# Performance work log

Hardware: AMD Instinct MI355X
Metric: run time of the kernel (lower is better)

The kernel has to match this reference:

```python
import jax, jax.numpy as jnp
import numpy as np
from jax import lax

LATENT = 128
CODEBOOK = 1024

def _conv(x, w, b):
    # NCHW conv, kernel OIHW, stride 1, padding 1 (same)
    y = lax.conv_general_dilated(x, w, (1, 1), ((1, 1), (1, 1)),
                                 dimension_numbers=('NCHW', 'OIHW', 'NCHW'))
    return y + b[None, :, None, None]

def _conv_transpose(x, w, b):
    # ConvTranspose2d(k=3, s=1, p=1) == conv with flipped kernel, in/out swapped, pad 1
    w_eff = jnp.flip(w, (2, 3)).transpose(1, 0, 2, 3)  # [Cin,Cout,3,3] -> [Cout,Cin,3,3]
    return _conv(x, w_eff, b)

def _maxpool2(x):
    return lax.reduce_window(x, -jnp.inf, lax.max, (1, 1, 2, 2), (1, 1, 2, 2), 'VALID')

def _upsample2(x):
    # F.interpolate(scale_factor=2), default nearest
    return jnp.repeat(jnp.repeat(x, 2, axis=2), 2, axis=3)

def setup_inputs() -> dict:
    key = jax.random.key(0)
    ks = jax.random.split(key, 20)
    f = jnp.float32
    inp = {
        'x': jax.random.uniform(ks[0], (8192, 1, 24, 24), dtype=f),
        'conv1_w': jax.random.normal(ks[1], (32, 1, 3, 3), f) * 0.1,
        'conv1_b': jnp.zeros((32,), f),
        'conv2_w': jax.random.normal(ks[2], (64, 32, 3, 3), f) * 0.05,
        'conv2_b': jnp.zeros((64,), f),
        'conv3_w': jax.random.normal(ks[3], (128, 64, 3, 3), f) * 0.04,
        'conv3_b': jnp.zeros((128,), f),
        'enc_fc_w': jax.random.normal(ks[4], (LATENT, 3 * 3 * 128), f) * 0.03,
        'enc_fc_b': jnp.zeros((LATENT,), f),
        'codebook': jax.random.normal(ks[5], (CODEBOOK, LATENT), f),
        'dec_fc_w': jax.random.normal(ks[6], (3 * 3 * 128, LATENT), f) * 0.09,
        'dec_fc_b': jnp.zeros((3 * 3 * 128,), f),
        'dct1_w': jax.random.normal(ks[7], (128, 64, 3, 3), f) * 0.03,  # [Cin,Cout,kh,kw]
        'dct1_b': jnp.zeros((64,), f),
        'dct2_w': jax.random.normal(ks[8], (64, 32, 3, 3), f) * 0.04,
        'dct2_b': jnp.zeros((32,), f),
        'dct3_w': jax.random.normal(ks[9], (32, 1, 3, 3), f) * 0.06,
        'dct3_b': jnp.zeros((1,), f),
    }
    return inp

def reference(x, conv1_w, conv1_b, conv2_w, conv2_b, conv3_w, conv3_b,
              enc_fc_w, enc_fc_b, codebook, dec_fc_w, dec_fc_b,
              dct1_w, dct1_b, dct2_w, dct2_b, dct3_w, dct3_b):
    # ---- Encoder ----
    h = _maxpool2(jax.nn.relu(_conv(x, conv1_w, conv1_b)))     # [B,32,12,12]
    h = _maxpool2(jax.nn.relu(_conv(h, conv2_w, conv2_b)))     # [B,64,6,6]
    h = _maxpool2(jax.nn.relu(_conv(h, conv3_w, conv3_b)))     # [B,128,3,3]
    z = h.reshape(-1, 3 * 3 * 128) @ enc_fc_w.T + enc_fc_b     # [B,128]
    # ---- Quantize (L2 nearest-codeword; matmul-trick distances, same argmin) ----
    d2 = (jnp.sum(z * z, axis=1, keepdims=True)
          - 2.0 * z @ codebook.T
          + jnp.sum(codebook * codebook, axis=1)[None, :])     # [B,K]
    idx = jnp.argmin(d2, axis=1)                               # [B]
    z_q = codebook[idx]                                        # [B,128]
    # ---- Decoder ----
    d = z_q @ dec_fc_w.T + dec_fc_b                            # [B,1152]
    d = d.reshape(-1, 128, 3, 3)
    d = _upsample2(jax.nn.relu(_conv_transpose(d, dct1_w, dct1_b)))  # [B,64,6,6]
    d = _upsample2(jax.nn.relu(_conv_transpose(d, dct2_w, dct2_b)))  # [B,32,12,12]
    d = _upsample2(jax.nn.relu(_conv_transpose(d, dct3_w, dct3_b)))  # [B,1,24,24]
    return d
```

## Files before the change

kernel.cpp:

```cpp
#include <hip/hip_runtime.h>

typedef __attribute__((ext_vector_type(8))) short short8;
typedef __attribute__((ext_vector_type(4))) float f32x4;
typedef unsigned short ushort_t;
typedef unsigned int uint_t;

#define OFF_W1R   0
#define OFF_BD2F  288
#define OFF_BD1F  18720
#define OFF_EWT   (18720+73728)
#define OFF_CT    (92448+147456)
#define OFF_CC    (239904+131072)
#define OFF_DWT   (370976+1024)
#define OFF_D1R   (372000+147456)
#define OFF_D3R   (593184+18432)
#define WS_WEIGHTS (611616+288)
#define OFF_W2BF  WS_WEIGHTS
#define OFF_W3BF  (OFF_W2BF+18432)
#define OFF_H     (OFF_W3BF+73728)
#define OFF_TABLE OFF_H
#define OFF_IDSN  (OFF_H+8192*1152)

__device__ __forceinline__ ushort_t f2bf(float v) {
  uint_t u = __float_as_uint(v);
  return (ushort_t)((u + 0x7FFFu + ((u >> 16) & 1u)) >> 16);
}
__device__ __forceinline__ float bf2f(ushort_t b) {
  return __uint_as_float(((uint_t)b) << 16);
}

#define P2_N (92160 + 294912 + 262144 + 73728 + 18432)
#define PREP_N (WS_WEIGHTS + P2_N)
__global__ void vq_prep_all(const float* __restrict__ conv1_w, const float* __restrict__ conv2_w,
                            const float* __restrict__ conv3_w, const float* __restrict__ enc_fc_w,
                            const float* __restrict__ codebook, const float* __restrict__ dec_fc_w,
                            const float* __restrict__ dct1_w, const float* __restrict__ dct2_w,
                            const float* __restrict__ dct3_w, float* __restrict__ ws) {
  int i0 = blockIdx.x * blockDim.x + threadIdx.x;
  if (i0 >= PREP_N) return;
  if (i0 < WS_WEIGHTS) {
    int i = i0;
    if (i < OFF_BD2F) {
      int tap = i >> 5, co = i & 31;
      ws[i] = conv1_w[co*9 + tap];
    } else if (i < OFF_CC) {
      return;
    } else if (i < OFF_DWT) {
      int k = i - OFF_CC;
      float s = 0.f;
      for (int j = 0; j < 128; ++j) { float v = codebook[k*128+j]; s += v*v; }
      ws[i] = s;
    } else if (i < OFF_D1R) {
      int l = i - OFF_DWT;
      int j = l % 1152, k = l / 1152;
      ws[i] = dec_fc_w[j*128 + k];
    } else if (i < OFF_D3R) {
      return;
    } else {
      int l = i - OFF_D3R;
      int tap = l % 9, ci = l / 9;
      ws[i] = dct3_w[ci*9 + (8 - tap)];
    }
    return;
  }
  int i = i0 - WS_WEIGHTS;
  ushort_t* W2  = (ushort_t*)(ws + OFF_W2BF);
  ushort_t* W3  = (ushort_t*)(ws + OFF_W3BF);
  ushort_t* EW  = (ushort_t*)(ws + OFF_EWT);
  ushort_t* CB  = (ushort_t*)(ws + OFF_CT);
  ushort_t* BD1 = (ushort_t*)(ws + OFF_BD1F);
  ushort_t* BD2 = (ushort_t*)(ws + OFF_BD2F);
  if (i < 18432) {
    int tap = i >> 11, r = i & 2047, co = r >> 5, ch = r & 31;
    float v = conv2_w[(co*32 + ch)*9 + tap];
    ushort_t hb = f2bf(v);
    W2[i] = hb; W2[18432 + i] = f2bf(v - bf2f(hb));
  } else if (i < 92160) {
    int j = i - 18432;
    int tap = j >> 13, r = j & 8191, co = r >> 6, ch = r & 63;
    float v = conv3_w[(co*64 + ch)*9 + tap];
    ushort_t hb = f2bf(v);
    W3[j] = hb; W3[73728 + j] = f2bf(v - bf2f(hb));
  } else if (i < 387072) {
    int r = i - 92160;
    int p = r / 147456; r %= 147456;
    int kk = r & 31, n = (r >> 5) & 127, ks = r >> 12;
    float v = enc_fc_w[n*1152 + ks*32 + kk];
    ushort_t hb = f2bf(v);
    if (p == 0) EW[r] = hb; else EW[147456 + r] = f2bf(v - bf2f(hb));
  } else if (i < 649216) {
    int r = i - 387072;
    int p = r / 131072; r %= 131072;
    int kk = r & 31, cw = (r >> 5) & 1023, ks = r >> 15;
    float v = codebook[cw*128 + ks*32 + kk];
    ushort_t hb = f2bf(v);
    if (p == 0) CB[r] = hb; else CB[131072 + r] = f2bf(v - bf2f(hb));
  } else if (i < 722944) {
    int r = i - 649216;
    int co = r / 1152, k = r - co*1152;
    int tap = k >> 7, ci = k & 127;
    float v = dct1_w[(ci*64 + co)*9 + (8 - tap)];
    ushort_t hb = f2bf(v);
    BD1[r] = hb; BD1[73728 + r] = f2bf(v - bf2f(hb));
  } else {
    int r = i - 722944;
    int co = r / 576, k = r - co*576;
    int tap = k >> 6, ci = k & 63;
    float v = dct2_w[(ci*32 + co)*9 + (8 - tap)];
    ushort_t hb = f2bf(v);
    BD2[r] = hb; BD2[18432 + r] = f2bf(v - bf2f(hb));
  }
}

__global__ __launch_bounds__(256, 4) void vq_enc(
    const float* __restrict__ x,
    const float* __restrict__ b1, const float* __restrict__ b2, const float* __restrict__ b3,
    const float* __restrict__ ws, ushort_t* __restrict__ hhi, ushort_t* __restrict__ hlo)
{
  __shared__ ushort_t R0h[7840], R0l[7840];
  __shared__ float XT[624];
  ushort_t* C3h = R0h;
  ushort_t* C3l = R0l;
  const int t = threadIdx.x;
  const int b = blockIdx.x;

  for (int i = t; i < 3920; i += 256) { ((uint_t*)R0h)[i] = 0u; ((uint_t*)R0l)[i] = 0u; }
  const float* xb = x + (size_t)b * 576;
  for (int i = t; i < 624; i += 256) {
    int row = i / 26, col = i - row * 26;
    XT[i] = (col >= 1 && col <= 24) ? xb[row*24 + col - 1] : 0.f;
  }
  __syncthreads();

  {
    int co = t & 31, g = t >> 5, gy = g >> 1, gx = g & 1;
    float w[9];
    #pragma unroll
    for (int k = 0; k < 9; ++k) w[k] = ws[OFF_W1R + k*32 + co];
    float bias = b1[co];
    #pragma unroll
    for (int pr = 0; pr < 3; ++pr) {
      int Y = gy*6 + pr*2;
      float a0[12], a1[12];
      #pragma unroll
      for (int i = 0; i < 12; ++i) { a0[i] = 0.f; a1[i] = 0.f; }
      #pragma unroll
      for (int wy = 0; wy < 4; ++wy) {
        int ry = Y - 1 + wy;
        if (ry < 0 || ry > 23) continue;
        const float2* rp = (const float2*)&XT[ry*26 + gx*12];
        float r[14];
        #pragma unroll
        for (int k = 0; k < 7; ++k) { float2 p = rp[k]; r[2*k] = p.x; r[2*k+1] = p.y; }
        if (wy < 3) {
          #pragma unroll
          for (int xx = 0; xx < 12; ++xx)
            #pragma unroll
            for (int dx = 0; dx < 3; ++dx) a0[xx] += r[xx+dx] * w[wy*3+dx];
        }
        if (wy >= 1) {
          #pragma unroll
          for (int xx = 0; xx < 12; ++xx)
            #pragma unroll
            for (int dx = 0; dx < 3; ++dx) a1[xx] += r[xx+dx] * w[(wy-1)*3+dx];
        }
      }
      #pragma unroll
      for (int pc = 0; pc < 6; ++pc) {
        float m = fmaxf(fmaxf(a0[2*pc], a0[2*pc+1]), fmaxf(a1[2*pc], a1[2*pc+1]));
        float v = m + bias; v = v > 0.f ? v : 0.f;
        int row = gy*3 + pr, colp = gx*6 + pc;
        int addr = ((row+1)*14 + (colp+1))*40 + co;
        ushort_t hb = f2bf(v);
        R0h[addr] = hb;
        R0l[addr] = f2bf(v - bf2f(hb));
      }
    }
  }
  __syncthreads();

  const int lane = t & 63, quad = lane >> 4, col = lane & 15;
  const int wv = t >> 6;

  {
    const int h = wv & 1, p = wv >> 1;
    const ushort_t* W2 = (const ushort_t*)(ws + OFF_W2BF);
    int baseA[5];
    #pragma unroll
    for (int mi = 0; mi < 5; ++mi) {
      int m = (h*5 + mi)*16 + col; if (m > 143) m = 143;
      int cell = m >> 2, sub = m & 3;
      int opy = cell / 6, opx = cell - opy*6;
      int y = 2*opy + (sub >> 1), xx = 2*opx + (sub & 1);
      baseA[mi] = (y*14 + xx)*40 + quad*8;
    }
    f32x4 acc[5][2];
    #pragma unroll
    for (int mi = 0; mi < 5; ++mi) { acc[mi][0] = (f32x4)0.f; acc[mi][1] = (f32x4)0.f; }
    const int co0 = p*32 + col, co1 = co0 + 16;
    #pragma unroll
    for (int t9 = 0; t9 < 9; ++t9) {
      const int TAPOFF = ((t9/3)*14 + (t9%3))*40;
      int bidx = t9*2048 + quad*8;
      short8 Bh0 = *(const short8*)(W2 + bidx + co0*32);
      short8 Bh1 = *(const short8*)(W2 + bidx + co1*32);
      short8 Bl0 = *(const short8*)(W2 + 18432 + bidx + co0*32);
      short8 Bl1 = *(const short8*)(W2 + 18432 + bidx + co1*32);
      #pragma unroll
      for (int mi = 0; mi < 5; ++mi) {
        int a = baseA[mi] + TAPOFF;
        short8 Ah = *(const short8*)(R0h + a);
        short8 Al = *(const short8*)(R0l + a);
        acc[mi][0] = __builtin_amdgcn_mfma_f32_16x16x32_bf16(Al, Bh0, acc[mi][0], 0, 0, 0);
        acc[mi][0] = __builtin_amdgcn_mfma_f32_16x16x32_bf16(Ah, Bl0, acc[mi][0], 0, 0, 0);
        acc[mi][0] = __builtin_amdgcn_mfma_f32_16x16x32_bf16(Ah, Bh0, acc[mi][0], 0, 0, 0);
        acc[mi][1] = __builtin_amdgcn_mfma_f32_16x16x32_bf16(Al, Bh1, acc[mi][1], 0, 0, 0);
        acc[mi][1] = __builtin_amdgcn_mfma_f32_16x16x32_bf16(Ah, Bl1, acc[mi][1], 0, 0, 0);
        acc[mi][1] = __builtin_amdgcn_mfma_f32_16x16x32_bf16(Ah, Bh1, acc[mi][1], 0, 0, 0);
      }
    }
    __syncthreads();
    for (int i = t; i < 2304; i += 256) { ((uint_t*)C3h)[i] = 0u; ((uint_t*)C3l)[i] = 0u; }
    __syncthreads();
    #pragma unroll
    for (int mi = 0; mi < 5; ++mi) {
      int cell = (h*5 + mi)*4 + quad;
      if (cell < 36) {
        int opy = cell / 6, opx = cell - opy*6;
        int wa = ((opy+1)*8 + (opx+1))*72;
        #pragma unroll
        for (int j = 0; j < 2; ++j) {
          int ch = j ? co1 : co0;
          f32x4 a = acc[mi][j];
          float v = fmaxf(fmaxf(a.x, a.y), fmaxf(a.z, a.w)) + b2[ch];
          v = v > 0.f ? v : 0.f;
          ushort_t hb = f2bf(v);
          C3h[wa + ch] = hb;
          C3l[wa + ch] = f2bf(v - bf2f(hb));
        }
      }
    }
  }
  __syncthreads();

  {
    const ushort_t* W3 = (const ushort_t*)(ws + OFF_W3BF);
    int baseA[3];
    #pragma unroll
    for (int mt = 0; mt < 3; ++mt) {
      int m = mt*16 + col; if (m > 35) m = 35;
      int cell = m >> 2, sub = m & 3;
      int opy = cell / 3, opx = cell - opy*3;
      int y = 2*opy + (sub >> 1), xx = 2*opx + (sub & 1);
      baseA[mt] = (y*8 + xx)*72 + quad*8;
    }
    f32x4 acc[3][2];
    #pragma unroll
    for (int mt = 0; mt < 3; ++mt) { acc[mt][0] = (f32x4)0.f; acc[mt][1] = (f32x4)0.f; }
    const int co0 = wv*16 + col, co1 = co0 + 64;
    #pragma unroll
    for (int ks = 0; ks < 18; ++ks) {
      const int t9 = ks >> 1, ch0 = (ks & 1)*32;
      const int TAPOFF = ((t9/3)*8 + (t9%3))*72;
      int bidx = t9*8192 + ch0 + quad*8;
      short8 Bh0 = *(const short8*)(W3 + bidx + co0*64);
      short8 Bh1 = *(const short8*)(W3 + bidx + co1*64);
      short8 Bl0 = *(const short8*)(W3 + 73728 + bidx + co0*64);
      short8 Bl1 = *(const short8*)(W3 + 73728 + bidx + co1*64);
      #pragma unroll
      for (int mt = 0; mt < 3; ++mt) {
        int a = baseA[mt] + TAPOFF + ch0;
        short8 Ah = *(const short8*)(C3h + a);
        short8 Al = *(const short8*)(C3l + a);
        acc[mt][0] = __builtin_amdgcn_mfma_f32_16x16x32_bf16(Al, Bh0, acc[mt][0], 0, 0, 0);
        acc[mt][0] = __builtin_amdgcn_mfma_f32_16x16x32_bf16(Ah, Bl0, acc[mt][0], 0, 0, 0);
        acc[mt][0] = __builtin_amdgcn_mfma_f32_16x16x32_bf16(Ah, Bh0, acc[mt][0], 0, 0, 0);
        acc[mt][1] = __builtin_amdgcn_mfma_f32_16x16x32_bf16(Al, Bh1, acc[mt][1], 0, 0, 0);
        acc[mt][1] = __builtin_amdgcn_mfma_f32_16x16x32_bf16(Ah, Bl1, acc[mt][1], 0, 0, 0);
        acc[mt][1] = __builtin_amdgcn_mfma_f32_16x16x32_bf16(Ah, Bh1, acc[mt][1], 0, 0, 0);
      }
    }
    ushort_t* hb_ = hhi + (size_t)b * 1152;
    ushort_t* lb_ = hlo + (size_t)b * 1152;
    #pragma unroll
    for (int mt = 0; mt < 3; ++mt) {
      int cell = mt*4 + quad;
      if (cell < 9) {
        #pragma unroll
        for (int j = 0; j < 2; ++j) {
          int ch = j ? co1 : co0;
          f32x4 a = acc[mt][j];
          float v = fmaxf(fmaxf(a.x, a.y), fmaxf(a.z, a.w)) + b3[ch];
          v = v > 0.f ? v : 0.f;
          ushort_t hb2 = f2bf(v);
          hb_[ch*9 + cell] = hb2;
          lb_[ch*9 + cell] = f2bf(v - bf2f(hb2));
        }
      }
    }
  }
}

__global__ __launch_bounds__(256, 4) void vq_fc_argmin(
    const float* __restrict__ efb, const float* __restrict__ ws,
    const ushort_t* __restrict__ hhi, const ushort_t* __restrict__ hlo,
    int* __restrict__ ids)
{
  __shared__ float ZL[16*132];
  __shared__ float WVs[64];
  __shared__ int   WIs[64];
  const int t = threadIdx.x;
  const int sb = blockIdx.x * 16;
  const int lane = t & 63, wv = t >> 6;
  const int col = lane & 15, quad = lane >> 4;

  const ushort_t* EW  = (const ushort_t*)(ws + OFF_EWT);
  const ushort_t* CBB = (const ushort_t*)(ws + OFF_CT);

  f32x4 acc0 = (f32x4)0.f, acc1 = (f32x4)0.f;
  const size_t hrow = (size_t)(sb + col) * 1152 + quad*8;
  #pragma unroll 4
  for (int ks = 0; ks < 36; ++ks) {
    short8 Ah = *(const short8*)(hhi + hrow + ks*32);
    short8 Al = *(const short8*)(hlo + hrow + ks*32);
    int n0 = wv*32 + col, n1 = n0 + 16;
    const ushort_t* bp0 = EW + (ks*128 + n0)*32 + quad*8;
    const ushort_t* bp1 = EW + (ks*128 + n1)*32 + quad*8;
    short8 Bh0 = *(const short8*)(bp0);
    short8 Bl0 = *(const short8*)(bp0 + 147456);
    short8 Bh1 = *(const short8*)(bp1);
    short8 Bl1 = *(const short8*)(bp1 + 147456);
    acc0 = __builtin_amdgcn_mfma_f32_16x16x32_bf16(Al, Bh0, acc0, 0, 0, 0);
    acc0 = __builtin_amdgcn_mfma_f32_16x16x32_bf16(Ah, Bl0, acc0, 0, 0, 0);
    acc0 = __builtin_amdgcn_mfma_f32_16x16x32_bf16(Ah, Bh0, acc0, 0, 0, 0);
    acc1 = __builtin_amdgcn_mfma_f32_16x16x32_bf16(Al, Bh1, acc1, 0, 0, 0);
    acc1 = __builtin_amdgcn_mfma_f32_16x16x32_bf16(Ah, Bl1, acc1, 0, 0, 0);
    acc1 = __builtin_amdgcn_mfma_f32_16x16x32_bf16(Ah, Bh1, acc1, 0, 0, 0);
  }
  {
    int n0 = wv*32 + col, n1 = n0 + 16;
    float bs0 = efb[n0], bs1 = efb[n1];
    #pragma unroll
    for (int r = 0; r < 4; ++r) {
      int m = quad*4 + r;
      ZL[m*132 + n0] = acc0[r] + bs0;
      ZL[m*132 + n1] = acc1[r] + bs1;
    }
  }
  __syncthreads();

  short8 zAh[4], zAl[4];
  #pragma unroll
  for (int ks = 0; ks < 4; ++ks) {
    const float* zp = &ZL[col*132 + ks*32 + quad*8];
    float4 z0 = *(const float4*)zp;
    float4 z1 = *(const float4*)(zp + 4);
    float zv[8] = {z0.x, z0.y, z0.z, z0.w, z1.x, z1.y, z1.z, z1.w};
    ushort_t ph[8], pl[8];
    #pragma unroll
    for (int e = 0; e < 8; ++e) {
      ushort_t hb = f2bf(zv[e]);
      ph[e] = hb; pl[e] = f2bf(zv[e] - bf2f(hb));
    }
    zAh[ks] = *(const short8*)ph;
    zAl[ks] = *(const short8*)pl;
  }

  float bestv[4]; int besti[4];
  #pragma unroll
  for (int r = 0; r < 4; ++r) { bestv[r] = 3.4e38f; besti[r] = 0; }
  for (int c4 = 0; c4 < 4; ++c4) {
    f32x4 dacc[4];
    #pragma unroll
    for (int nn = 0; nn < 4; ++nn) dacc[nn] = (f32x4)0.f;
    #pragma unroll
    for (int ks = 0; ks < 4; ++ks) {
      #pragma unroll
      for (int nn = 0; nn < 4; ++nn) {
        int cw = (wv*16 + c4*4 + nn)*16 + col;
        const ushort_t* bp = CBB + (size_t)(ks*1024 + cw)*32 + quad*8;
        short8 Bh = *(const short8*)bp;
        short8 Bl = *(const short8*)(bp + 131072);
        dacc[nn] = __builtin_amdgcn_mfma_f32_16x16x32_bf16(zAl[ks], Bh, dacc[nn], 0, 0, 0);
        dacc[nn] = __builtin_amdgcn_mfma_f32_16x16x32_bf16(zAh[ks], Bl, dacc[nn], 0, 0, 0);
        dacc[nn] = __builtin_amdgcn_mfma_f32_16x16x32_bf16(zAh[ks], Bh, dacc[nn], 0, 0, 0);
      }
    }
    #pragma unroll
    for (int nn = 0; nn < 4; ++nn) {
      int cw = (wv*16 + c4*4 + nn)*16 + col;
      float ccv = ws[OFF_CC + cw];
      #pragma unroll
      for (int r = 0; r < 4; ++r) {
        float dist = ccv - 2.f*dacc[nn][r];
        if (dist < bestv[r]) { bestv[r] = dist; besti[r] = cw; }
      }
    }
  }

  #pragma unroll
  for (int r = 0; r < 4; ++r) {
    float v = bestv[r]; int ii = besti[r];
    #pragma unroll
    for (int off = 8; off >= 1; off >>= 1) {
      float v2 = __shfl_xor(v, off); int i2 = __shfl_xor(ii, off);
      if (v2 < v || (v2 == v && i2 < ii)) { v = v2; ii = i2; }
    }
    if (col == 0) {
      int m = quad*4 + r;
      WVs[wv*16 + m] = v; WIs[wv*16 + m] = ii;
    }
  }
  __syncthreads();
  if (t < 16) {
    float v = WVs[t]; int ii = WIs[t];
    #pragma unroll
    for (int w2 = 1; w2 < 4; ++w2) {
      float v2 = WVs[w2*16 + t]; int i2 = WIs[w2*16 + t];
      if (v2 < v || (v2 == v && i2 < ii)) { v = v2; ii = i2; }
    }
    ids[sb + t] = ii;
  }
}

__global__ __launch_bounds__(256, 4) void vq_dec_table(
    const float* __restrict__ codebook, const float* __restrict__ decb,
    const float* __restrict__ d1b, const float* __restrict__ d2b, const float* __restrict__ d3b,
    const float* __restrict__ ws, float* __restrict__ table)
{
  __shared__ float POOL[8008];
  __shared__ float PS[1536];
  __shared__ float ZQ[128];
  ushort_t* FAh = (ushort_t*)POOL;
  ushort_t* FAl = FAh + 3400;
  ushort_t* GAh = (ushort_t*)(POOL + 3400);
  ushort_t* GAl = GAh + 4608;
  float* R2 = POOL;

  const int t = threadIdx.x;
  const int cw = blockIdx.x;
  const int lane = t & 63, wv = t >> 6;
  const int col = lane & 15, quad = lane >> 4;

  for (int i = t; i < 8008; i += 256) POOL[i] = 0.f;
  if (t < 128) ZQ[t] = codebook[(size_t)cw*128 + t];
  __syncthreads();

  #pragma unroll
  for (int p = 0; p < 5; ++p) {
    int j = t + p*256;
    if (j < 1152) {
      float a0 = decb[j];
      const float* wb = ws + OFF_DWT + j;
      #pragma unroll 4
      for (int k = 0; k < 128; ++k) a0 += wb[k*1152] * ZQ[k];
      int ci = j / 9, rem = j - ci*9;
      int pix = ((rem/3)+1)*5 + (rem%3) + 1;
      ushort_t hb = f2bf(a0);
      FAh[pix*136 + ci] = hb;
      FAl[pix*136 + ci] = f2bf(a0 - bf2f(hb));
    }
  }
  __syncthreads();

  const ushort_t* BD1 = (const ushort_t*)(ws + OFF_BD1F);
  f32x4 acc1 = (f32x4)0.f;
  {
    const int m9 = col < 9 ? col : 8;
    const int oy = m9/3, ox = m9 - oy*3;
    const int co = wv*16 + col;
    #pragma unroll 4
    for (int ks = 0; ks < 36; ++ks) {
      int kb = ks*32 + quad*8;
      int tap = kb >> 7, ci0 = kb & 127;
      int pix = (oy + tap/3)*5 + ox + tap%3;
      short8 Ah = *(const short8*)(FAh + pix*136 + ci0);
      short8 Al = *(const short8*)(FAl + pix*136 + ci0);
      const ushort_t* bp = BD1 + co*1152 + kb;
      short8 Bh = *(const short8*)bp;
      short8 Bl = *(const short8*)(bp + 73728);
      acc1 = __builtin_amdgcn_mfma_f32_16x16x32_bf16(Al, Bh, acc1, 0, 0, 0);
      acc1 = __builtin_amdgcn_mfma_f32_16x16x32_bf16(Ah, Bl, acc1, 0, 0, 0);
      acc1 = __builtin_amdgcn_mfma_f32_16x16x32_bf16(Ah, Bh, acc1, 0, 0, 0);
    }
  }
  {
    const int co = wv*16 + col;
    float bias = d1b[co];
    #pragma unroll
    for (int r = 0; r < 4; ++r) {
      int m = quad*4 + r;
      if (m < 9) {
        int oy = m/3, ox = m - oy*3;
        float v = acc1[r] + bias; v = v > 0.f ? v : 0.f;
        ushort_t hb = f2bf(v), lb = f2bf(v - bf2f(hb));
        int rbase = (2*oy+1)*8 + (2*ox+1);
        GAh[(rbase  )*72 + co] = hb; GAh[(rbase+1)*72 + co] = hb;
        GAh[(rbase+8)*72 + co] = hb; GAh[(rbase+9)*72 + co] = hb;
        GAl[(rbase  )*72 + co] = lb; GAl[(rbase+1)*72 + co] = lb;
        GAl[(rbase+8)*72 + co] = lb; GAl[(rbase+9)*72 + co] = lb;
      }
    }
  }
  __syncthreads();

  const ushort_t* BD2 = (const ushort_t*)(ws + OFF_BD2F);
  f32x4 acc2[3];
  acc2[0] = (f32x4)0.f; acc2[1] = (f32x4)0.f; acc2[2] = (f32x4)0.f;
  const int h = wv >> 1, js = (wv & 1)*3;
  for (int ks = h*9; ks < h*9 + 9; ++ks) {
    int kb = ks*32 + quad*8;
    int tap = kb >> 6, ci0 = kb & 63;
    int ty = tap/3, tx = tap - ty*3;
    #pragma unroll
    for (int jj = 0; jj < 3; ++jj) {
      int job = js + jj;
      int mt = job >> 1, nt = job & 1;
      int m = mt*16 + col; if (m > 35) m = 35;
      int oy = m/6, ox = m - oy*6;
      int pix = (oy+ty)*8 + ox+tx;
      short8 Ah = *(const short8*)(GAh + pix*72 + ci0);
      short8 Al = *(const short8*)(GAl + pix*72 + ci0);
      int co = nt*16 + col;
      const ushort_t* bp = BD2 + co*576 + kb;
      short8 Bh = *(const short8*)bp;
      short8 Bl = *(const short8*)(bp + 18432);
      acc2[jj] = __builtin_amdgcn_mfma_f32_16x16x32_bf16(Al, Bh, acc2[jj], 0, 0, 0);
      acc2[jj] = __builtin_amdgcn_mfma_f32_16x16x32_bf16(Ah, Bl, acc2[jj], 0, 0, 0);
      acc2[jj] = __builtin_amdgcn_mfma_f32_16x16x32_bf16(Ah, Bh, acc2[jj], 0, 0, 0);
    }
  }
  __syncthreads();
  if (h == 1) {
    #pragma unroll
    for (int jj = 0; jj < 3; ++jj) {
      int job = js + jj;
      #pragma unroll
      for (int r = 0; r < 4; ++r) PS[(job*64 + lane)*4 + r] = acc2[jj][r];
    }
  }
  for (int i = t; i < 6468; i += 256) R2[i] = 0.f;
  __syncthreads();
  if (h == 0) {
    #pragma unroll
    for (int jj = 0; jj < 3; ++jj) {
      int job = js + jj;
      int mt = job >> 1, nt = job & 1;
      int co = nt*16 + col;
      float bias = d2b[co];
      #pragma unroll
      for (int r = 0; r < 4; ++r) {
        float v = acc2[jj][r] + PS[(job*64 + lane)*4 + r];
        int m = mt*16 + quad*4 + r;
        if (m < 36) {
          int oy = m/6, ox = m - oy*6;
          v += bias; v = v > 0.f ? v : 0.f;
          int rbase = (2*oy+1)*14 + (2*ox+1);
          R2[(rbase   )*33 + co] = v; R2[(rbase+ 1)*33 + co] = v;
          R2[(rbase+14)*33 + co] = v; R2[(rbase+15)*33 + co] = v;
        }
      }
    }
  }
  __syncthreads();

  if (t < 144) {
    int yy = t / 12, xx = t - yy*12;
    const float* w3 = ws + OFF_D3R;
    float acc = d3b[0];
    #pragma unroll
    for (int dy = 0; dy < 3; ++dy)
      #pragma unroll
      for (int dx = 0; dx < 3; ++dx) {
        const float* rp = &R2[((yy+dy)*14 + xx+dx)*33];
        const float* wp = w3 + dy*3 + dx;
        #pragma unroll 8
        for (int ci = 0; ci < 32; ++ci) acc += rp[ci] * wp[ci*9];
      }
    float v = acc > 0.f ? acc : 0.f;
    float* ob = table + (size_t)cw * 576;
    int o0 = (2*yy)*24 + 2*xx;
    ob[o0] = v; ob[o0+1] = v; ob[o0+24] = v; ob[o0+25] = v;
  }
}

__global__ __launch_bounds__(256, 8) void vq_scatter(
    const float* __restrict__ table, const int* __restrict__ ids,
    float* __restrict__ out, int nvec)
{
  int idx = blockIdx.x * 256 + threadIdx.x;
  if (idx >= nvec) return;
  int b = idx / 144;
  int r = idx - b * 144;
  int cw = ids[b];
  ((float4*)out)[idx] = ((const float4*)(table + (size_t)cw * 576))[r];
}

extern "C" void kernel_launch(void* const* d_in, const int* in_sizes, int n_in,
                              void* d_out, int out_size, void* d_ws, size_t ws_size,
                              hipStream_t stream) {
  const float* x   = (const float*)d_in[0];
  const float* c1w = (const float*)d_in[1];
  const float* c1b = (const float*)d_in[2];
  const float* c2w = (const float*)d_in[3];
  const float* c2b = (const float*)d_in[4];
  const float* c3w = (const float*)d_in[5];
  const float* c3b = (const float*)d_in[6];
  const float* efw = (const float*)d_in[7];
  const float* efb = (const float*)d_in[8];
  const float* cb  = (const float*)d_in[9];
  const float* dfw = (const float*)d_in[10];
  const float* dfb = (const float*)d_in[11];
  const float* dw1 = (const float*)d_in[12];
  const float* db1 = (const float*)d_in[13];
  const float* dw2 = (const float*)d_in[14];
  const float* db2 = (const float*)d_in[15];
  const float* dw3 = (const float*)d_in[16];
  const float* db3 = (const float*)d_in[17];
  float* ws = (float*)d_ws;
  ushort_t* hhi  = (ushort_t*)(ws + OFF_H);
  ushort_t* hlo  = hhi + (size_t)8192*1152;
  float* table = ws + OFF_TABLE;
  int*   ids   = (int*)(ws + OFF_IDSN);
  float* outp = (float*)d_out;
  int B = in_sizes[0] / 576;

  vq_prep_all<<<(PREP_N + 255) / 256, 256, 0, stream>>>(c1w, c2w, c3w, efw, cb, dfw, dw1, dw2, dw3, ws);
  vq_enc<<<B, 256, 0, stream>>>(x, c1b, c2b, c3b, ws, hhi, hlo);
  vq_fc_argmin<<<B/16, 256, 0, stream>>>(efb, ws, hhi, hlo, ids);
  vq_dec_table<<<1024, 256, 0, stream>>>(cb, dfb, db1, db2, db3, ws, table);
  int nvec = B * 144;
  vq_scatter<<<(nvec + 255) / 256, 256, 0, stream>>>(table, ids, outp, nvec);
}
```

Before: 627.4 us.

## Fuse decoder table into encoder launch and merge argmin with output scatter

The encoder kernel and the codebook decoder-table kernel are merged into one launch: the first 1024 blocks build the per-codeword decoded images, and the remaining blocks run the encoder. This lets the two independent stages run concurrently and share the GPU. The argmin kernel now handles 32 samples per block and writes the output directly by copying the selected table rows, which removes the separate scatter kernel and the global ids buffer. In exchange, shared memory is unioned across both roles, the table moves to its own workspace region, and the argmin kernel does more work per block.

```diff
diff --git a/kernel.cpp b/kernel.cpp
--- a/kernel.cpp
+++ b/kernel.cpp
@@ -18,8 +18,7 @@
 #define OFF_W2BF  WS_WEIGHTS
 #define OFF_W3BF  (OFF_W2BF+18432)
 #define OFF_H     (OFF_W3BF+73728)
-#define OFF_TABLE OFF_H
-#define OFF_IDSN  (OFF_H+8192*1152)
+#define OFF_TABLE (OFF_H + 8192*1152)
 
 __device__ __forceinline__ ushort_t f2bf(float v) {
   uint_t u = __float_as_uint(v);
@@ -112,267 +111,450 @@
   }
 }
 
-__global__ __launch_bounds__(256, 4) void vq_enc(
+#define DECB 1024
+__global__ __launch_bounds__(256, 4) void vq_enc_dec(
     const float* __restrict__ x,
     const float* __restrict__ b1, const float* __restrict__ b2, const float* __restrict__ b3,
-    const float* __restrict__ ws, ushort_t* __restrict__ hhi, ushort_t* __restrict__ hlo)
+    const float* __restrict__ codebook, const float* __restrict__ decb,
+    const float* __restrict__ d1b, const float* __restrict__ d2b, const float* __restrict__ d3b,
+    const float* __restrict__ ws, ushort_t* __restrict__ hhi, ushort_t* __restrict__ hlo,
+    float* __restrict__ table)
 {
-  __shared__ ushort_t R0h[7840], R0l[7840];
-  __shared__ float XT[624];
-  ushort_t* C3h = R0h;
-  ushort_t* C3l = R0l;
+  __shared__ __align__(16) char SMEM[38688];
   const int t = threadIdx.x;
-  const int b = blockIdx.x;
-
-  for (int i = t; i < 3920; i += 256) { ((uint_t*)R0h)[i] = 0u; ((uint_t*)R0l)[i] = 0u; }
-  const float* xb = x + (size_t)b * 576;
-  for (int i = t; i < 624; i += 256) {
-    int row = i / 26, col = i - row * 26;
-    XT[i] = (col >= 1 && col <= 24) ? xb[row*24 + col - 1] : 0.f;
-  }
-  __syncthreads();
+  const int lane = t & 63, wv = t >> 6;
+  const int col = lane & 15, quad = lane >> 4;
+
+  if (blockIdx.x >= DECB) {
+    ushort_t* R0h = (ushort_t*)SMEM;
+    ushort_t* R0l = R0h + 7840;
+    float*    XT  = (float*)(SMEM + 31360);
+    ushort_t* C3h = R0h;
+    ushort_t* C3l = R0l;
+    const int b = blockIdx.x - DECB;
+
+    for (int i = t; i < 3920; i += 256) { ((uint_t*)R0h)[i] = 0u; ((uint_t*)R0l)[i] = 0u; }
+    const float* xb = x + (size_t)b * 576;
+    for (int i = t; i < 624; i += 256) {
+      int row = i / 26, c = i - row * 26;
+      XT[i] = (c >= 1 && c <= 24) ? xb[row*24 + c - 1] : 0.f;
+    }
+    __syncthreads();
+
+    {
+      int co = t & 31, g = t >> 5, gy = g >> 1, gx = g & 1;
+      float w[9];
+      #pragma unroll
+      for (int k = 0; k < 9; ++k) w[k] = ws[OFF_W1R + k*32 + co];
+      float bias = b1[co];
+      #pragma unroll
+      for (int pr = 0; pr < 3; ++pr) {
+        int Y = gy*6 + pr*2;
+        float a0[12], a1[12];
+        #pragma unroll
+        for (int i = 0; i < 12; ++i) { a0[i] = 0.f; a1[i] = 0.f; }
+        #pragma unroll
+        for (int wy = 0; wy < 4; ++wy) {
+          int ry = Y - 1 + wy;
+          if (ry < 0 || ry > 23) continue;
+          const float2* rp = (const float2*)&XT[ry*26 + gx*12];
+          float r[14];
+          #pragma unroll
+          for (int k = 0; k < 7; ++k) { float2 p = rp[k]; r[2*k] = p.x; r[2*k+1] = p.y; }
+          if (wy < 3) {
+            #pragma unroll
+            for (int xx = 0; xx < 12; ++xx)
+              #pragma unroll
+              for (int dx = 0; dx < 3; ++dx) a0[xx] += r[xx+dx] * w[wy*3+dx];
+          }
+          if (wy >= 1) {
+            #pragma unroll
+            for (int xx = 0; xx < 12; ++xx)
+              #pragma unroll
+              for (int dx = 0; dx < 3; ++dx) a1[xx] += r[xx+dx] * w[(wy-1)*3+dx];
+          }
+        }
+        #pragma unroll
+        for (int pc = 0; pc < 6; ++pc) {
+          float m = fmaxf(fmaxf(a0[2*pc], a0[2*pc+1]), fmaxf(a1[2*pc], a1[2*pc+1]));
+          float v = m + bias; v = v > 0.f ? v : 0.f;
+          int row = gy*3 + pr, colp = gx*6 + pc;
+          int addr = ((row+1)*14 + (colp+1))*40 + co;
+          ushort_t hb = f2bf(v);
+          R0h[addr] = hb;
+          R0l[addr] = f2bf(v - bf2f(hb));
+        }
+      }
+    }
+    __syncthreads();
+
+    {
+      const int h = wv & 1, p = wv >> 1;
+      const ushort_t* W2 = (const ushort_t*)(ws + OFF_W2BF);
+      int baseA[5];
+      #pragma unroll
+      for (int mi = 0; mi < 5; ++mi) {
+        int m = (h*5 + mi)*16 + col; if (m > 143) m = 143;
+        int cell = m >> 2, sub = m & 3;
+        int opy = cell / 6, opx = cell - opy*6;
+        int y = 2*opy + (sub >> 1), xx = 2*opx + (sub & 1);
+        baseA[mi] = (y*14 + xx)*40 + quad*8;
+      }
+      f32x4 acc[5][2];
+      #pragma unroll
+      for (int mi = 0; mi < 5; ++mi) { acc[mi][0] = (f32x4)0.f; acc[mi][1] = (f32x4)0.f; }
+      const int co0 = p*32 + col, co1 = co0 + 16;
+      #pragma unroll
+      for (int t9 = 0; t9 < 9; ++t9) {
+        const int TAPOFF = ((t9/3)*14 + (t9%3))*40;
+        int bidx = t9*2048 + quad*8;
+        short8 Bh0 = *(const short8*)(W2 + bidx + co0*32);
+        short8 Bh1 = *(const short8*)(W2 + bidx + co1*32);
+        short8 Bl0 = *(const short8*)(W2 + 18432 + bidx + co0*32);
+        short8 Bl1 = *(const short8*)(W2 + 18432 + bidx + co1*32);
+        #pragma unroll
+        for (int mi = 0; mi < 5; ++mi) {
+          int a = baseA[mi] + TAPOFF;
+          short8 Ah = *(const short8*)(R0h + a);
+          short8 Al = *(const short8*)(R0l + a);
+          acc[mi][0] = __builtin_amdgcn_mfma_f32_16x16x32_bf16(Al, Bh0, acc[mi][0], 0, 0, 0);
+          acc[mi][0] = __builtin_amdgcn_mfma_f32_16x16x32_bf16(Ah, Bl0, acc[mi][0], 0, 0, 0);
+          acc[mi][0] = __builtin_amdgcn_mfma_f32_16x16x32_bf16(Ah, Bh0, acc[mi][0], 0, 0, 0);
+          acc[mi][1] = __builtin_amdgcn_mfma_f32_16x16x32_bf16(Al, Bh1, acc[mi][1], 0, 0, 0);
+          acc[mi][1] = __builtin_amdgcn_mfma_f32_16x16x32_bf16(Ah, Bl1, acc[mi][1], 0, 0, 0);
+          acc[mi][1] = __builtin_amdgcn_mfma_f32_16x16x32_bf16(Ah, Bh1, acc[mi][1], 0, 0, 0);
+        }
+      }
+      __syncthreads();
+      for (int i = t; i < 2304; i += 256) { ((uint_t*)C3h)[i] = 0u; ((uint_t*)C3l)[i] = 0u; }
+      __syncthreads();
+      #pragma unroll
+      for (int mi = 0; mi < 5; ++mi) {
+        int cell = (h*5 + mi)*4 + quad;
+        if (cell < 36) {
+          int opy = cell / 6, opx = cell - opy*6;
+          int wa = ((opy+1)*8 + (opx+1))*72;
+          #pragma unroll
+          for (int j = 0; j < 2; ++j) {
+            int ch = j ? co1 : co0;
+            f32x4 a = acc[mi][j];
+            float v = fmaxf(fmaxf(a.x, a.y), fmaxf(a.z, a.w)) + b2[ch];
+            v = v > 0.f ? v : 0.f;
+            ushort_t hb = f2bf(v);
+            C3h[wa + ch] = hb;
+            C3l[wa + ch] = f2bf(v - bf2f(hb));
+          }
+        }
+      }
+    }
+    __syncthreads();
+
+    {
+      const ushort_t* W3 = (const ushort_t*)(ws + OFF_W3BF);
+      int baseA[3];
+      #pragma unroll
+      for (int mt = 0; mt < 3; ++mt) {
+        int m = mt*16 + col; if (m > 35) m = 35;
+        int cell = m >> 2, sub = m & 3;
+        int opy = cell / 3, opx = cell - opy*3;
+        int y = 2*opy + (sub >> 1), xx = 2*opx + (sub & 1);
+        baseA[mt] = (y*8 + xx)*72 + quad*8;
+      }
+      f32x4 acc[3][2];
+      #pragma unroll
+      for (int mt = 0; mt < 3; ++mt) { acc[mt][0] = (f32x4)0.f; acc[mt][1] = (f32x4)0.f; }
+      const int co0 = wv*16 + col, co1 = co0 + 64;
+      #pragma unroll
+      for (int ks = 0; ks < 18; ++ks) {
+        const int t9 = ks >> 1, ch0 = (ks & 1)*32;
+        const int TAPOFF = ((t9/3)*8 + (t9%3))*72;
+        int bidx = t9*8192 + ch0 + quad*8;
+        short8 Bh0 = *(const short8*)(W3 + bidx + co0*64);
+        short8 Bh1 = *(const short8*)(W3 + bidx + co1*64);
+        short8 Bl0 = *(const short8*)(W3 + 73728 + bidx + co0*64);
+        short8 Bl1 = *(const short8*)(W3 + 73728 + bidx + co1*64);
+        #pragma unroll
+        for (int mt = 0; mt < 3; ++mt) {
+          int a = baseA[mt] + TAPOFF + ch0;
+          short8 Ah = *(const short8*)(C3h + a);
+          short8 Al = *(const short8*)(C3l + a);
+          acc[mt][0] = __builtin_amdgcn_mfma_f32_16x16x32_bf16(Al, Bh0, acc[mt][0], 0, 0, 0);
+          acc[mt][0] = __builtin_amdgcn_mfma_f32_16x16x32_bf16(Ah, Bl0, acc[mt][0], 0, 0, 0);
+          acc[mt][0] = __builtin_amdgcn_mfma_f32_16x16x32_bf16(Ah, Bh0, acc[mt][0], 0, 0, 0);
+          acc[mt][1] = __builtin_amdgcn_mfma_f32_16x16x32_bf16(Al, Bh1, acc[mt][1], 0, 0, 0);
+          acc[mt][1] = __builtin_amdgcn_mfma_f32_16x16x32_bf16(Ah, Bl1, acc[mt][1], 0, 0, 0);
+          acc[mt][1] = __builtin_amdgcn_mfma_f32_16x16x32_bf16(Ah, Bh1, acc[mt][1], 0, 0, 0);
+        }
+      }
+      ushort_t* hb_ = hhi + (size_t)b * 1152;
+      ushort_t* lb_ = hlo + (size_t)b * 1152;
+      #pragma unroll
+      for (int mt = 0; mt < 3; ++mt) {
+        int cell = mt*4 + quad;
+        if (cell < 9) {
+          #pragma unroll
+          for (int j = 0; j < 2; ++j) {
+            int ch = j ? co1 : co0;
+            f32x4 a = acc[mt][j];
+            float v = fmaxf(fmaxf(a.x, a.y), fmaxf(a.z, a.w)) + b3[ch];
+            v = v > 0.f ? v : 0.f;
+            ushort_t hb2 = f2bf(v);
+            hb_[ch*9 + cell] = hb2;
+            lb_[ch*9 + cell] = f2bf(v - bf2f(hb2));
+          }
+        }
+      }
+    }
+    return;
+  }
 
   {
-    int co = t & 31, g = t >> 5, gy = g >> 1, gx = g & 1;
-    float w[9];
-    #pragma unroll
-    for (int k = 0; k < 9; ++k) w[k] = ws[OFF_W1R + k*32 + co];
-    float bias = b1[co];
-    #pragma unroll
-    for (int pr = 0; pr < 3; ++pr) {
-      int Y = gy*6 + pr*2;
-      float a0[12], a1[12];
-      #pragma unroll
-      for (int i = 0; i < 12; ++i) { a0[i] = 0.f; a1[i] = 0.f; }
-      #pragma unroll
-      for (int wy = 0; wy < 4; ++wy) {
-        int ry = Y - 1 + wy;
-        if (ry < 0 || ry > 23) continue;
-        const float2* rp = (const float2*)&XT[ry*26 + gx*12];
-        float r[14];
-        #pragma unroll
-        for (int k = 0; k < 7; ++k) { float2 p = rp[k]; r[2*k] = p.x; r[2*k+1] = p.y; }
-        if (wy < 3) {
-          #pragma unroll
-          for (int xx = 0; xx < 12; ++xx)
-            #pragma unroll
-            for (int dx = 0; dx < 3; ++dx) a0[xx] += r[xx+dx] * w[wy*3+dx];
-        }
-        if (wy >= 1) {
-          #pragma unroll
-          for (int xx = 0; xx < 12; ++xx)
-            #pragma unroll
-            for (int dx = 0; dx < 3; ++dx) a1[xx] += r[xx+dx] * w[(wy-1)*3+dx];
-        }
-      }
-      #pragma unroll
-      for (int pc = 0; pc < 6; ++pc) {
-        float m = fmaxf(fmaxf(a0[2*pc], a0[2*pc+1]), fmaxf(a1[2*pc], a1[2*pc+1]));
-        float v = m + bias; v = v > 0.f ? v : 0.f;
-        int row = gy*3 + pr, colp = gx*6 + pc;
-        int addr = ((row+1)*14 + (colp+1))*40 + co;
-        ushort_t hb = f2bf(v);
-        R0h[addr] = hb;
-        R0l[addr] = f2bf(v - bf2f(hb));
-      }
-    }
-  }
-  __syncthreads();
-
-  const int lane = t & 63, quad = lane >> 4, col = lane & 15;
-  const int wv = t >> 6;
-
-  {
-    const int h = wv & 1, p = wv >> 1;
-    const ushort_t* W2 = (const ushort_t*)(ws + OFF_W2BF);
-    int baseA[5];
-    #pragma unroll
-    for (int mi = 0; mi < 5; ++mi) {
-      int m = (h*5 + mi)*16 + col; if (m > 143) m = 143;
-      int cell = m >> 2, sub = m & 3;
-      int opy = cell / 6, opx = cell - opy*6;
-      int y = 2*opy + (sub >> 1), xx = 2*opx + (sub & 1);
-      baseA[mi] = (y*14 + xx)*40 + quad*8;
-    }
-    f32x4 acc[5][2];
-    #pragma unroll
-    for (int mi = 0; mi < 5; ++mi) { acc[mi][0] = (f32x4)0.f; acc[mi][1] = (f32x4)0.f; }
-    const int co0 = p*32 + col, co1 = co0 + 16;
-    #pragma unroll
-    for (int t9 = 0; t9 < 9; ++t9) {
-      const int TAPOFF = ((t9/3)*14 + (t9%3))*40;
-      int bidx = t9*2048 + quad*8;
-      short8 Bh0 = *(const short8*)(W2 + bidx + co0*32);
-      short8 Bh1 = *(const short8*)(W2 + bidx + co1*32);
-      short8 Bl0 = *(const short8*)(W2 + 18432 + bidx + co0*32);
-      short8 Bl1 = *(const short8*)(W2 + 18432 + bidx + co1*32);
-      #pragma unroll
-      for (int mi = 0; mi < 5; ++mi) {
-        int a = baseA[mi] + TAPOFF;
-        short8 Ah = *(const short8*)(R0h + a);
-        short8 Al = *(const short8*)(R0l + a);
-        acc[mi][0] = __builtin_amdgcn_mfma_f32_16x16x32_bf16(Al, Bh0, acc[mi][0], 0, 0, 0);
-        acc[mi][0] = __builtin_amdgcn_mfma_f32_16x16x32_bf16(Ah, Bl0, acc[mi][0], 0, 0, 0);
-        acc[mi][0] = __builtin_amdgcn_mfma_f32_16x16x32_bf16(Ah, Bh0, acc[mi][0], 0, 0, 0);
-        acc[mi][1] = __builtin_amdgcn_mfma_f32_16x16x32_bf16(Al, Bh1, acc[mi][1], 0, 0, 0);
-        acc[mi][1] = __builtin_amdgcn_mfma_f32_16x16x32_bf16(Ah, Bl1, acc[mi][1], 0, 0, 0);
-        acc[mi][1] = __builtin_amdgcn_mfma_f32_16x16x32_bf16(Ah, Bh1, acc[mi][1], 0, 0, 0);
-      }
-    }
-    __syncthreads();
-    for (int i = t; i < 2304; i += 256) { ((uint_t*)C3h)[i] = 0u; ((uint_t*)C3l)[i] = 0u; }
-    __syncthreads();
-    #pragma unroll
-    for (int mi = 0; mi < 5; ++mi) {
-      int cell = (h*5 + mi)*4 + quad;
-      if (cell < 36) {
-        int opy = cell / 6, opx = cell - opy*6;
-        int wa = ((opy+1)*8 + (opx+1))*72;
-        #pragma unroll
-        for (int j = 0; j < 2; ++j) {
-          int ch = j ? co1 : co0;
-          f32x4 a = acc[mi][j];
-          float v = fmaxf(fmaxf(a.x, a.y), fmaxf(a.z, a.w)) + b2[ch];
-          v = v > 0.f ? v : 0.f;
-          ushort_t hb = f2bf(v);
-          C3h[wa + ch] = hb;
-          C3l[wa + ch] = f2bf(v - bf2f(hb));
-        }
-      }
-    }
-  }
-  __syncthreads();
-
-  {
-    const ushort_t* W3 = (const ushort_t*)(ws + OFF_W3BF);
-    int baseA[3];
-    #pragma unroll
-    for (int mt = 0; mt < 3; ++mt) {
-      int m = mt*16 + col; if (m > 35) m = 35;
-      int cell = m >> 2, sub = m & 3;
-      int opy = cell / 3, opx = cell - opy*3;
-      int y = 2*opy + (sub >> 1), xx = 2*opx + (sub & 1);
-      baseA[mt] = (y*8 + xx)*72 + quad*8;
-    }
-    f32x4 acc[3][2];
-    #pragma unroll
-    for (int mt = 0; mt < 3; ++mt) { acc[mt][0] = (f32x4)0.f; acc[mt][1] = (f32x4)0.f; }
-    const int co0 = wv*16 + col, co1 = co0 + 64;
-    #pragma unroll
-    for (int ks = 0; ks < 18; ++ks) {
-      const int t9 = ks >> 1, ch0 = (ks & 1)*32;
-      const int TAPOFF = ((t9/3)*8 + (t9%3))*72;
-      int bidx = t9*8192 + ch0 + quad*8;
-      short8 Bh0 = *(const short8*)(W3 + bidx + co0*64);
-      short8 Bh1 = *(const short8*)(W3 + bidx + co1*64);
-      short8 Bl0 = *(const short8*)(W3 + 73728 + bidx + co0*64);
-      short8 Bl1 = *(const short8*)(W3 + 73728 + bidx + co1*64);
-      #pragma unroll
-      for (int mt = 0; mt < 3; ++mt) {
-        int a = baseA[mt] + TAPOFF + ch0;
-        short8 Ah = *(const short8*)(C3h + a);
-        short8 Al = *(const short8*)(C3l + a);
-        acc[mt][0] = __builtin_amdgcn_mfma_f32_16x16x32_bf16(Al, Bh0, acc[mt][0], 0, 0, 0);
-        acc[mt][0] = __builtin_amdgcn_mfma_f32_16x16x32_bf16(Ah, Bl0, acc[mt][0], 0, 0, 0);
-        acc[mt][0] = __builtin_amdgcn_mfma_f32_16x16x32_bf16(Ah, Bh0, acc[mt][0], 0, 0, 0);
-        acc[mt][1] = __builtin_amdgcn_mfma_f32_16x16x32_bf16(Al, Bh1, acc[mt][1], 0, 0, 0);
-        acc[mt][1] = __builtin_amdgcn_mfma_f32_16x16x32_bf16(Ah, Bl1, acc[mt][1], 0, 0, 0);
-        acc[mt][1] = __builtin_amdgcn_mfma_f32_16x16x32_bf16(Ah, Bh1, acc[mt][1], 0, 0, 0);
-      }
-    }
-    ushort_t* hb_ = hhi + (size_t)b * 1152;
-    ushort_t* lb_ = hlo + (size_t)b * 1152;
-    #pragma unroll
-    for (int mt = 0; mt < 3; ++mt) {
-      int cell = mt*4 + quad;
-      if (cell < 9) {
-        #pragma unroll
-        for (int j = 0; j < 2; ++j) {
-          int ch = j ? co1 : co0;
-          f32x4 a = acc[mt][j];
-          float v = fmaxf(fmaxf(a.x, a.y), fmaxf(a.z, a.w)) + b3[ch];
-          v = v > 0.f ? v : 0.f;
-          ushort_t hb2 = f2bf(v);
-          hb_[ch*9 + cell] = hb2;
-          lb_[ch*9 + cell] = f2bf(v - bf2f(hb2));
-        }
-      }
+    float* POOL = (float*)SMEM;
+    float* PS   = (float*)(SMEM + 32032);
+    float* ZQ   = (float*)(SMEM + 38176);
+    ushort_t* FAh = (ushort_t*)POOL;
+    ushort_t* FAl = FAh + 3400;
+    ushort_t* GAh = (ushort_t*)(POOL + 3400);
+    ushort_t* GAl = GAh + 4608;
+    float* R2 = POOL;
+    const int cw = blockIdx.x;
+
+    for (int i = t; i < 8008; i += 256) POOL[i] = 0.f;
+    if (t < 128) ZQ[t] = codebook[(size_t)cw*128 + t];
+    __syncthreads();
+
+    #pragma unroll
+    for (int p = 0; p < 5; ++p) {
+      int j = t + p*256;
+      if (j < 1152) {
+        float a0 = decb[j];
+        const float* wb = ws + OFF_DWT + j;
+        #pragma unroll 4
+        for (int k = 0; k < 128; ++k) a0 += wb[k*1152] * ZQ[k];
+        int ci = j / 9, rem = j - ci*9;
+        int pix = ((rem/3)+1)*5 + (rem%3) + 1;
+        ushort_t hb = f2bf(a0);
+        FAh[pix*136 + ci] = hb;
+        FAl[pix*136 + ci] = f2bf(a0 - bf2f(hb));
+      }
+    }
+    __syncthreads();
+
+    const ushort_t* BD1 = (const ushort_t*)(ws + OFF_BD1F);
+    f32x4 acc1 = (f32x4)0.f;
+    {
+      const int m9 = col < 9 ? col : 8;
+      const int oy = m9/3, ox = m9 - oy*3;
+      const int co = wv*16 + col;
+      #pragma unroll 4
+      for (int ks = 0; ks < 36; ++ks) {
+        int kb = ks*32 + quad*8;
+        int tap = kb >> 7, ci0 = kb & 127;
+        int pix = (oy + tap/3)*5 + ox + tap%3;
+        short8 Ah = *(const short8*)(FAh + pix*136 + ci0);
+        short8 Al = *(const short8*)(FAl + pix*136 + ci0);
+        const ushort_t* bp = BD1 + co*1152 + kb;
+        short8 Bh = *(const short8*)bp;
+        short8 Bl = *(const short8*)(bp + 73728);
+        acc1 = __builtin_amdgcn_mfma_f32_16x16x32_bf16(Al, Bh, acc1, 0, 0, 0);
+        acc1 = __builtin_amdgcn_mfma_f32_16x16x32_bf16(Ah, Bl, acc1, 0, 0, 0);
+        acc1 = __builtin_amdgcn_mfma_f32_16x16x32_bf16(Ah, Bh, acc1, 0, 0, 0);
+      }
+    }
+    {
+      const int co = wv*16 + col;
+      float bias = d1b[co];
+      #pragma unroll
+      for (int r = 0; r < 4; ++r) {
+        int m = quad*4 + r;
+        if (m < 9) {
+          int oy = m/3, ox = m - oy*3;
+          float v = acc1[r] + bias; v = v > 0.f ? v : 0.f;
+          ushort_t hb = f2bf(v), lb = f2bf(v - bf2f(hb));
+          int rbase = (2*oy+1)*8 + (2*ox+1);
+          GAh[(rbase  )*72 + co] = hb; GAh[(rbase+1)*72 + co] = hb;
+          GAh[(rbase+8)*72 + co] = hb; GAh[(rbase+9)*72 + co] = hb;
+          GAl[(rbase  )*72 + co] = lb; GAl[(rbase+1)*72 + co] = lb;
+          GAl[(rbase+8)*72 + co] = lb; GAl[(rbase+9)*72 + co] = lb;
+        }
+      }
+    }
+    __syncthreads();
+
+    const ushort_t* BD2 = (const ushort_t*)(ws + OFF_BD2F);
+    f32x4 acc2[3];
+    acc2[0] = (f32x4)0.f; acc2[1] = (f32x4)0.f; acc2[2] = (f32x4)0.f;
+    const int h = wv >> 1, js = (wv & 1)*3;
+    for (int ks = h*9; ks < h*9 + 9; ++ks) {
+      int kb = ks*32 + quad*8;
+      int tap = kb >> 6, ci0 = kb & 63;
+      int ty = tap/3, tx = tap - ty*3;
+      #pragma unroll
+      for (int jj = 0; jj < 3; ++jj) {
+        int job = js + jj;
+        int mt = job >> 1, nt = job & 1;
+        int m = mt*16 + col; if (m > 35) m = 35;
+        int oy = m/6, ox = m - oy*6;
+        int pix = (oy+ty)*8 + ox+tx;
+        short8 Ah = *(const short8*)(GAh + pix*72 + ci0);
+        short8 Al = *(const short8*)(GAl + pix*72 + ci0);
+        int co = nt*16 + col;
+        const ushort_t* bp = BD2 + co*576 + kb;
+        short8 Bh = *(const short8*)bp;
+        short8 Bl = *(const short8*)(bp + 18432);
+        acc2[jj] = __builtin_amdgcn_mfma_f32_16x16x32_bf16(Al, Bh, acc2[jj], 0, 0, 0);
+        acc2[jj] = __builtin_amdgcn_mfma_f32_16x16x32_bf16(Ah, Bl, acc2[jj], 0, 0, 0);
+        acc2[jj] = __builtin_amdgcn_mfma_f32_16x16x32_bf16(Ah, Bh, acc2[jj], 0, 0, 0);
+      }
+    }
+    __syncthreads();
+    if (h == 1) {
+      #pragma unroll
+      for (int jj = 0; jj < 3; ++jj) {
+        int job = js + jj;
+        #pragma unroll
+        for (int r = 0; r < 4; ++r) PS[(job*64 + lane)*4 + r] = acc2[jj][r];
+      }
+    }
+    for (int i = t; i < 6468; i += 256) R2[i] = 0.f;
+    __syncthreads();
+    if (h == 0) {
+      #pragma unroll
+      for (int jj = 0; jj < 3; ++jj) {
+        int job = js + jj;
+        int mt = job >> 1, nt = job & 1;
+        int co = nt*16 + col;
+        float bias = d2b[co];
+        #pragma unroll
+        for (int r = 0; r < 4; ++r) {
+          float v = acc2[jj][r] + PS[(job*64 + lane)*4 + r];
+          int m = mt*16 + quad*4 + r;
+          if (m < 36) {
+            int oy = m/6, ox = m - oy*6;
+            v += bias; v = v > 0.f ? v : 0.f;
+            int rbase = (2*oy+1)*14 + (2*ox+1);
+            R2[(rbase   )*33 + co] = v; R2[(rbase+ 1)*33 + co] = v;
+            R2[(rbase+14)*33 + co] = v; R2[(rbase+15)*33 + co] = v;
+          }
+        }
+      }
+    }
+    __syncthreads();
+
+    if (t < 144) {
+      int yy = t / 12, xx = t - yy*12;
+      const float* w3 = ws + OFF_D3R;
+      float acc = d3b[0];
+      #pragma unroll
+      for (int dy = 0; dy < 3; ++dy)
+        #pragma unroll
+        for (int dx = 0; dx < 3; ++dx) {
+          const float* rp = &R2[((yy+dy)*14 + xx+dx)*33];
+          const float* wp = w3 + dy*3 + dx;
+          #pragma unroll 8
+          for (int ci = 0; ci < 32; ++ci) acc += rp[ci] * wp[ci*9];
+        }
+      float v = acc > 0.f ? acc : 0.f;
+      float* ob = table + (size_t)cw * 576;
+      int o0 = (2*yy)*24 + 2*xx;
+      ob[o0] = v; ob[o0+1] = v; ob[o0+24] = v; ob[o0+25] = v;
     }
   }
 }
 
-__global__ __launch_bounds__(256, 4) void vq_fc_argmin(
+__global__ __launch_bounds__(256, 2) void vq_fc_argmin_scatter(
     const float* __restrict__ efb, const float* __restrict__ ws,
     const ushort_t* __restrict__ hhi, const ushort_t* __restrict__ hlo,
-    int* __restrict__ ids)
+    const float* __restrict__ table, float* __restrict__ out)
 {
-  __shared__ float ZL[16*132];
-  __shared__ float WVs[64];
-  __shared__ int   WIs[64];
+  __shared__ float ZL[32*132];
+  __shared__ float WVs[128];
+  __shared__ int   WIs[128];
+  __shared__ int   IDX[32];
   const int t = threadIdx.x;
-  const int sb = blockIdx.x * 16;
+  const int sb = blockIdx.x * 32;
   const int lane = t & 63, wv = t >> 6;
   const int col = lane & 15, quad = lane >> 4;
 
   const ushort_t* EW  = (const ushort_t*)(ws + OFF_EWT);
   const ushort_t* CBB = (const ushort_t*)(ws + OFF_CT);
 
-  f32x4 acc0 = (f32x4)0.f, acc1 = (f32x4)0.f;
-  const size_t hrow = (size_t)(sb + col) * 1152 + quad*8;
-  #pragma unroll 4
+  f32x4 acc[2][2];
+  acc[0][0] = (f32x4)0.f; acc[0][1] = (f32x4)0.f;
+  acc[1][0] = (f32x4)0.f; acc[1][1] = (f32x4)0.f;
+  const size_t hrow0 = (size_t)(sb + col) * 1152 + quad*8;
+  const size_t hrow1 = (size_t)(sb + 16 + col) * 1152 + quad*8;
+  const int n0 = wv*32 + col, n1 = n0 + 16;
+  #pragma unroll 2
   for (int ks = 0; ks < 36; ++ks) {
-    short8 Ah = *(const short8*)(hhi + hrow + ks*32);
-    short8 Al = *(const short8*)(hlo + hrow + ks*32);
-    int n0 = wv*32 + col, n1 = n0 + 16;
+    short8 Ah0 = *(const short8*)(hhi + hrow0 + ks*32);
+    short8 Al0 = *(const short8*)(hlo + hrow0 + ks*32);
+    short8 Ah1 = *(const short8*)(hhi + hrow1 + ks*32);
+    short8 Al1 = *(const short8*)(hlo + hrow1 + ks*32);
     const ushort_t* bp0 = EW + (ks*128 + n0)*32 + quad*8;
     const ushort_t* bp1 = EW + (ks*128 + n1)*32 + quad*8;
     short8 Bh0 = *(const short8*)(bp0);
     short8 Bl0 = *(const short8*)(bp0 + 147456);
     short8 Bh1 = *(const short8*)(bp1);
     short8 Bl1 = *(const short8*)(bp1 + 147456);
-    acc0 = __builtin_amdgcn_mfma_f32_16x16x32_bf16(Al, Bh0, acc0, 0, 0, 0);
-    acc0 = __builtin_amdgcn_mfma_f32_16x16x32_bf16(Ah, Bl0, acc0, 0, 0, 0);
-    acc0 = __builtin_amdgcn_mfma_f32_16x16x32_bf16(Ah, Bh0, acc0, 0, 0, 0);
-    acc1 = __builtin_amdgcn_mfma_f32_16x16x32_bf16(Al, Bh1, acc1, 0, 0, 0);
-    acc1 = __builtin_amdgcn_mfma_f32_16x16x32_bf16(Ah, Bl1, acc1, 0, 0, 0);
-    acc1 = __builtin_amdgcn_mfma_f32_16x16x32_bf16(Ah, Bh1, acc1, 0, 0, 0);
+    acc[0][0] = __builtin_amdgcn_mfma_f32_16x16x32_bf16(Al0, Bh0, acc[0][0], 0, 0, 0);
+    acc[0][0] = __builtin_amdgcn_mfma_f32_16x16x32_bf16(Ah0, Bl0, acc[0][0], 0, 0, 0);
+    acc[0][0] = __builtin_amdgcn_mfma_f32_16x16x32_bf16(Ah0, Bh0, acc[0][0], 0, 0, 0);
+    acc[0][1] = __builtin_amdgcn_mfma_f32_16x16x32_bf16(Al0, Bh1, acc[0][1], 0, 0, 0);
+    acc[0][1] = __builtin_amdgcn_mfma_f32_16x16x32_bf16(Ah0, Bl1, acc[0][1], 0, 0, 0);
+    acc[0][1] = __builtin_amdgcn_mfma_f32_16x16x32_bf16(Ah0, Bh1, acc[0][1], 0, 0, 0);
+    acc[1][0] = __builtin_amdgcn_mfma_f32_16x16x32_bf16(Al1, Bh0, acc[1][0], 0, 0, 0);
+    acc[1][0] = __builtin_amdgcn_mfma_f32_16x16x32_bf16(Ah1, Bl0, acc[1][0], 0, 0, 0);
+    acc[1][0] = __builtin_amdgcn_mfma_f32_16x16x32_bf16(Ah1, Bh0, acc[1][0], 0, 0, 0);
+    acc[1][1] = __builtin_amdgcn_mfma_f32_16x16x32_bf16(Al1, Bh1, acc[1][1], 0, 0, 0);
+    acc[1][1] = __builtin_amdgcn_mfma_f32_16x16x32_bf16(Ah1, Bl1, acc[1][1], 0, 0, 0);
+    acc[1][1] = __builtin_amdgcn_mfma_f32_16x16x32_bf16(Ah1, Bh1, acc[1][1], 0, 0, 0);
   }
   {
-    int n0 = wv*32 + col, n1 = n0 + 16;
     float bs0 = efb[n0], bs1 = efb[n1];
     #pragma unroll
-    for (int r = 0; r < 4; ++r) {
-      int m = quad*4 + r;
-      ZL[m*132 + n0] = acc0[r] + bs0;
-      ZL[m*132 + n1] = acc1[r] + bs1;
+    for (int m2 = 0; m2 < 2; ++m2) {
+      #pragma unroll
+      for (int r = 0; r < 4; ++r) {
+        int m = m2*16 + quad*4 + r;
+        ZL[m*132 + n0] = acc[m2][0][r] + bs0;
+        ZL[m*132 + n1] = acc[m2][1][r] + bs1;
+      }
     }
   }
   __syncthreads();
 
-  short8 zAh[4], zAl[4];
+  short8 zAh[2][4], zAl[2][4];
   #pragma unroll
-  for (int ks = 0; ks < 4; ++ks) {
-    const float* zp = &ZL[col*132 + ks*32 + quad*8];
-    float4 z0 = *(const float4*)zp;
-    float4 z1 = *(const float4*)(zp + 4);
-    float zv[8] = {z0.x, z0.y, z0.z, z0.w, z1.x, z1.y, z1.z, z1.w};
-    ushort_t ph[8], pl[8];
-    #pragma unroll
-    for (int e = 0; e < 8; ++e) {
-      ushort_t hb = f2bf(zv[e]);
-      ph[e] = hb; pl[e] = f2bf(zv[e] - bf2f(hb));
-    }
-    zAh[ks] = *(const short8*)ph;
-    zAl[ks] = *(const short8*)pl;
-  }
-
-  float bestv[4]; int besti[4];
+  for (int m2 = 0; m2 < 2; ++m2) {
+    #pragma unroll
+    for (int ks = 0; ks < 4; ++ks) {
+      const float* zp = &ZL[(m2*16 + col)*132 + ks*32 + quad*8];
+      float4 z0 = *(const float4*)zp;
+      float4 z1 = *(const float4*)(zp + 4);
+      float zv[8] = {z0.x, z0.y, z0.z, z0.w, z1.x, z1.y, z1.z, z1.w};
+      ushort_t ph[8], pl[8];
+      #pragma unroll
+      for (int e = 0; e < 8; ++e) {
+        ushort_t hb = f2bf(zv[e]);
+        ph[e] = hb; pl[e] = f2bf(zv[e] - bf2f(hb));
+      }
+      zAh[m2][ks] = *(const short8*)ph;
+      zAl[m2][ks] = *(const short8*)pl;
+    }
+  }
+
+  float bestv[2][4]; int besti[2][4];
   #pragma unroll
-  for (int r = 0; r < 4; ++r) { bestv[r] = 3.4e38f; besti[r] = 0; }
+  for (int m2 = 0; m2 < 2; ++m2)
+    #pragma unroll
+    for (int r = 0; r < 4; ++r) { bestv[m2][r] = 3.4e38f; besti[m2][r] = 0; }
   for (int c4 = 0; c4 < 4; ++c4) {
-    f32x4 dacc[4];
-    #pragma unroll
-    for (int nn = 0; nn < 4; ++nn) dacc[nn] = (f32x4)0.f;
+    f32x4 dacc[2][4];
+    #pragma unroll
+    for (int m2 = 0; m2 < 2; ++m2)
+      #pragma unroll
+      for (int nn = 0; nn < 4; ++nn) dacc[m2][nn] = (f32x4)0.f;
     #pragma unroll
     for (int ks = 0; ks < 4; ++ks) {
       #pragma unroll
@@ -381,9 +563,12 @@
         const ushort_t* bp = CBB + (size_t)(ks*1024 + cw)*32 + quad*8;
         short8 Bh = *(const short8*)bp;
         short8 Bl = *(const short8*)(bp + 131072);
-        dacc[nn] = __builtin_amdgcn_mfma_f32_16x16x32_bf16(zAl[ks], Bh, dacc[nn], 0, 0, 0);
-        dacc[nn] = __builtin_amdgcn_mfma_f32_16x16x32_bf16(zAh[ks], Bl, dacc[nn], 0, 0, 0);
-        dacc[nn] = __builtin_amdgcn_mfma_f32_16x16x32_bf16(zAh[ks], Bh, dacc[nn], 0, 0, 0);
+        #pragma unroll
+        for (int m2 = 0; m2 < 2; ++m2) {
+          dacc[m2][nn] = __builtin_amdgcn_mfma_f32_16x16x32_bf16(zAl[m2][ks], Bh, dacc[m2][nn], 0, 0, 0);
+          dacc[m2][nn] = __builtin_amdgcn_mfma_f32_16x16x32_bf16(zAh[m2][ks], Bl, dacc[m2][nn], 0, 0, 0);
+          dacc[m2][nn] = __builtin_amdgcn_mfma_f32_16x16x32_bf16(zAh[m2][ks], Bh, dacc[m2][nn], 0, 0, 0);
+        }
       }
     }
     #pragma unroll
@@ -391,209 +576,48 @@
       int cw = (wv*16 + c4*4 + nn)*16 + col;
       float ccv = ws[OFF_CC + cw];
       #pragma unroll
-      for (int r = 0; r < 4; ++r) {
-        float dist = ccv - 2.f*dacc[nn][r];
-        if (dist < bestv[r]) { bestv[r] = dist; besti[r] = cw; }
-      }
+      for (int m2 = 0; m2 < 2; ++m2)
+        #pragma unroll
+        for (int r = 0; r < 4; ++r) {
+          float dist = ccv - 2.f*dacc[m2][nn][r];
+          if (dist < bestv[m2][r]) { bestv[m2][r] = dist; besti[m2][r] = cw; }
+        }
     }
   }
 
   #pragma unroll
-  for (int r = 0; r < 4; ++r) {
-    float v = bestv[r]; int ii = besti[r];
-    #pragma unroll
-    for (int off = 8; off >= 1; off >>= 1) {
-      float v2 = __shfl_xor(v, off); int i2 = __shfl_xor(ii, off);
+  for (int m2 = 0; m2 < 2; ++m2)
+    #pragma unroll
+    for (int r = 0; r < 4; ++r) {
+      float v = bestv[m2][r]; int ii = besti[m2][r];
+      #pragma unroll
+      for (int off = 8; off >= 1; off >>= 1) {
+        float v2 = __shfl_xor(v, off); int i2 = __shfl_xor(ii, off);
+        if (v2 < v || (v2 == v && i2 < ii)) { v = v2; ii = i2; }
+      }
+      if (col == 0) {
+        int m = m2*16 + quad*4 + r;
+        WVs[wv*32 + m] = v; WIs[wv*32 + m] = ii;
+      }
+    }
+  __syncthreads();
+  if (t < 32) {
+    float v = WVs[t]; int ii = WIs[t];
+    #pragma unroll
+    for (int w2 = 1; w2 < 4; ++w2) {
+      float v2 = WVs[w2*32 + t]; int i2 = WIs[w2*32 + t];
       if (v2 < v || (v2 == v && i2 < ii)) { v = v2; ii = i2; }
     }
-    if (col == 0) {
-      int m = quad*4 + r;
-      WVs[wv*16 + m] = v; WIs[wv*16 + m] = ii;
-    }
+    IDX[t] = ii;
   }
   __syncthreads();
-  if (t < 16) {
-    float v = WVs[t]; int ii = WIs[t];
-    #pragma unroll
-    for (int w2 = 1; w2 < 4; ++w2) {
-      float v2 = WVs[w2*16 + t]; int i2 = WIs[w2*16 + t];
-      if (v2 < v || (v2 == v && i2 < ii)) { v = v2; ii = i2; }
-    }
-    ids[sb + t] = ii;
-  }
-}
-
-__global__ __launch_bounds__(256, 4) void vq_dec_table(
-    const float* __restrict__ codebook, const float* __restrict__ decb,
-    const float* __restrict__ d1b, const float* __restrict__ d2b, const float* __restrict__ d3b,
-    const float* __restrict__ ws, float* __restrict__ table)
-{
-  __shared__ float POOL[8008];
-  __shared__ float PS[1536];
-  __shared__ float ZQ[128];
-  ushort_t* FAh = (ushort_t*)POOL;
-  ushort_t* FAl = FAh + 3400;
-  ushort_t* GAh = (ushort_t*)(POOL + 3400);
-  ushort_t* GAl = GAh + 4608;
-  float* R2 = POOL;
-
-  const int t = threadIdx.x;
-  const int cw = blockIdx.x;
-  const int lane = t & 63, wv = t >> 6;
-  const int col = lane & 15, quad = lane >> 4;
-
-  for (int i = t; i < 8008; i += 256) POOL[i] = 0.f;
-  if (t < 128) ZQ[t] = codebook[(size_t)cw*128 + t];
-  __syncthreads();
-
-  #pragma unroll
-  for (int p = 0; p < 5; ++p) {
-    int j = t + p*256;
-    if (j < 1152) {
-      float a0 = decb[j];
-      const float* wb = ws + OFF_DWT + j;
-      #pragma unroll 4
-      for (int k = 0; k < 128; ++k) a0 += wb[k*1152] * ZQ[k];
-      int ci = j / 9, rem = j - ci*9;
-      int pix = ((rem/3)+1)*5 + (rem%3) + 1;
-      ushort_t hb = f2bf(a0);
-      FAh[pix*136 + ci] = hb;
-      FAl[pix*136 + ci] = f2bf(a0 - bf2f(hb));
-    }
-  }
-  __syncthreads();
-
-  const ushort_t* BD1 = (const ushort_t*)(ws + OFF_BD1F);
-  f32x4 acc1 = (f32x4)0.f;
-  {
-    const int m9 = col < 9 ? col : 8;
-    const int oy = m9/3, ox = m9 - oy*3;
-    const int co = wv*16 + col;
-    #pragma unroll 4
-    for (int ks = 0; ks < 36; ++ks) {
-      int kb = ks*32 + quad*8;
-      int tap = kb >> 7, ci0 = kb & 127;
-      int pix = (oy + tap/3)*5 + ox + tap%3;
-      short8 Ah = *(const short8*)(FAh + pix*136 + ci0);
-      short8 Al = *(const short8*)(FAl + pix*136 + ci0);
-      const ushort_t* bp = BD1 + co*1152 + kb;
-      short8 Bh = *(const short8*)bp;
-      short8 Bl = *(const short8*)(bp + 73728);
-      acc1 = __builtin_amdgcn_mfma_f32_16x16x32_bf16(Al, Bh, acc1, 0, 0, 0);
-      acc1 = __builtin_amdgcn_mfma_f32_16x16x32_bf16(Ah, Bl, acc1, 0, 0, 0);
-      acc1 = __builtin_amdgcn_mfma_f32_16x16x32_bf16(Ah, Bh, acc1, 0, 0, 0);
-    }
-  }
-  {
-    const int co = wv*16 + col;
-    float bias = d1b[co];
-    #pragma unroll
-    for (int r = 0; r < 4; ++r) {
-      int m = quad*4 + r;
-      if (m < 9) {
-        int oy = m/3, ox = m - oy*3;
-        float v = acc1[r] + bias; v = v > 0.f ? v : 0.f;
-        ushort_t hb = f2bf(v), lb = f2bf(v - bf2f(hb));
-        int rbase = (2*oy+1)*8 + (2*ox+1);
-        GAh[(rbase  )*72 + co] = hb; GAh[(rbase+1)*72 + co] = hb;
-        GAh[(rbase+8)*72 + co] = hb; GAh[(rbase+9)*72 + co] = hb;
-        GAl[(rbase  )*72 + co] = lb; GAl[(rbase+1)*72 + co] = lb;
-        GAl[(rbase+8)*72 + co] = lb; GAl[(rbase+9)*72 + co] = lb;
-      }
-    }
-  }
-  __syncthreads();
-
-  const ushort_t* BD2 = (const ushort_t*)(ws + OFF_BD2F);
-  f32x4 acc2[3];
-  acc2[0] = (f32x4)0.f; acc2[1] = (f32x4)0.f; acc2[2] = (f32x4)0.f;
-  const int h = wv >> 1, js = (wv & 1)*3;
-  for (int ks = h*9; ks < h*9 + 9; ++ks) {
-    int kb = ks*32 + quad*8;
-    int tap = kb >> 6, ci0 = kb & 63;
-    int ty = tap/3, tx = tap - ty*3;
-    #pragma unroll
-    for (int jj = 0; jj < 3; ++jj) {
-      int job = js + jj;
-      int mt = job >> 1, nt = job & 1;
-      int m = mt*16 + col; if (m > 35) m = 35;
-      int oy = m/6, ox = m - oy*6;
-      int pix = (oy+ty)*8 + ox+tx;
-      short8 Ah = *(const short8*)(GAh + pix*72 + ci0);
-      short8 Al = *(const short8*)(GAl + pix*72 + ci0);
-      int co = nt*16 + col;
-      const ushort_t* bp = BD2 + co*576 + kb;
-      short8 Bh = *(const short8*)bp;
-      short8 Bl = *(const short8*)(bp + 18432);
-      acc2[jj] = __builtin_amdgcn_mfma_f32_16x16x32_bf16(Al, Bh, acc2[jj], 0, 0, 0);
-      acc2[jj] = __builtin_amdgcn_mfma_f32_16x16x32_bf16(Ah, Bl, acc2[jj], 0, 0, 0);
-      acc2[jj] = __builtin_amdgcn_mfma_f32_16x16x32_bf16(Ah, Bh, acc2[jj], 0, 0, 0);
-    }
-  }
-  __syncthreads();
-  if (h == 1) {
-    #pragma unroll
-    for (int jj = 0; jj < 3; ++jj) {
-      int job = js + jj;
-      #pragma unroll
-      for (int r = 0; r < 4; ++r) PS[(job*64 + lane)*4 + r] = acc2[jj][r];
-    }
-  }
-  for (int i = t; i < 6468; i += 256) R2[i] = 0.f;
-  __syncthreads();
-  if (h == 0) {
-    #pragma unroll
-    for (int jj = 0; jj < 3; ++jj) {
-      int job = js + jj;
-      int mt = job >> 1, nt = job & 1;
-      int co = nt*16 + col;
-      float bias = d2b[co];
-      #pragma unroll
-      for (int r = 0; r < 4; ++r) {
-        float v = acc2[jj][r] + PS[(job*64 + lane)*4 + r];
-        int m = mt*16 + quad*4 + r;
-        if (m < 36) {
-          int oy = m/6, ox = m - oy*6;
-          v += bias; v = v > 0.f ? v : 0.f;
-          int rbase = (2*oy+1)*14 + (2*ox+1);
-          R2[(rbase   )*33 + co] = v; R2[(rbase+ 1)*33 + co] = v;
-          R2[(rbase+14)*33 + co] = v; R2[(rbase+15)*33 + co] = v;
-        }
-      }
-    }
-  }
-  __syncthreads();
-
-  if (t < 144) {
-    int yy = t / 12, xx = t - yy*12;
-    const float* w3 = ws + OFF_D3R;
-    float acc = d3b[0];
-    #pragma unroll
-    for (int dy = 0; dy < 3; ++dy)
-      #pragma unroll
-      for (int dx = 0; dx < 3; ++dx) {
-        const float* rp = &R2[((yy+dy)*14 + xx+dx)*33];
-        const float* wp = w3 + dy*3 + dx;
-        #pragma unroll 8
-        for (int ci = 0; ci < 32; ++ci) acc += rp[ci] * wp[ci*9];
-      }
-    float v = acc > 0.f ? acc : 0.f;
-    float* ob = table + (size_t)cw * 576;
-    int o0 = (2*yy)*24 + 2*xx;
-    ob[o0] = v; ob[o0+1] = v; ob[o0+24] = v; ob[o0+25] = v;
-  }
-}
-
-__global__ __launch_bounds__(256, 8) void vq_scatter(
-    const float* __restrict__ table, const int* __restrict__ ids,
-    float* __restrict__ out, int nvec)
-{
-  int idx = blockIdx.x * 256 + threadIdx.x;
-  if (idx >= nvec) return;
-  int b = idx / 144;
-  int r = idx - b * 144;
-  int cw = ids[b];
-  ((float4*)out)[idx] = ((const float4*)(table + (size_t)cw * 576))[r];
+
+  const float4* tb4 = (const float4*)table;
+  float4* out4 = (float4*)(out + (size_t)sb * 576);
+  for (int i = t; i < 32*144; i += 256) {
+    int s = i / 144, r = i - s*144;
+    out4[s*144 + r] = tb4[(size_t)IDX[s]*144 + r];
+  }
 }
 
 extern "C" void kernel_launch(void* const* d_in, const int* in_sizes, int n_in,
@@ -621,14 +645,11 @@
   ushort_t* hhi  = (ushort_t*)(ws + OFF_H);
   ushort_t* hlo  = hhi + (size_t)8192*1152;
   float* table = ws + OFF_TABLE;
-  int*   ids   = (int*)(ws + OFF_IDSN);
   float* outp = (float*)d_out;
   int B = in_sizes[0] / 576;
 
   vq_prep_all<<<(PREP_N + 255) / 256, 256, 0, stream>>>(c1w, c2w, c3w, efw, cb, dfw, dw1, dw2, dw3, ws);
-  vq_enc<<<B, 256, 0, stream>>>(x, c1b, c2b, c3b, ws, hhi, hlo);
-  vq_fc_argmin<<<B/16, 256, 0, stream>>>(efb, ws, hhi, hlo, ids);
-  vq_dec_table<<<1024, 256, 0, stream>>>(cb, dfb, db1, db2, db3, ws, table);
-  int nvec = B * 144;
-  vq_scatter<<<(nvec + 255) / 256, 256, 0, stream>>>(table, ids, outp, nvec);
+  vq_enc_dec<<<DECB + B, 256, 0, stream>>>(x, c1b, c2b, c3b, cb, dfb, db1, db2, db3,
+                                           ws, hhi, hlo, table);
+  vq_fc_argmin_scatter<<<B/32, 256, 0, stream>>>(efb, ws, hhi, hlo, table, outp);
 }
```

Result: faster. 605.4 us (-3.5%).
